# Optimization experiments

Hardware: AMD Instinct MI355X
Metric: run time of the kernel (lower is better)

## Reference

```python
import jax, jax.numpy as jnp
import numpy as np


def setup_inputs() -> dict:
    key = jax.random.key(0)
    feats = jax.random.normal(key, (16, 64, 128, 128), dtype=jnp.float32)
    return {"feats": feats, "stride": 2}


def reference(feats, stride):
    # Zero-insertion upsampling: equivalent to conv_transpose2d with an
    # s x s kernel whose only nonzero is at [0,0], stride=s, groups=C.
    # out[b,c,i*s,j*s] = feats[b,c,i,j]; all other entries are zero.
    B, C, H, W = feats.shape
    out = jnp.zeros((B, C, H * stride, W * stride), dtype=feats.dtype)
    out = out.at[:, :, ::stride, ::stride].set(feats)
    return out
```

## Files before the change

kernel.cpp:

```cpp
#include <hip/hip_runtime.h>


#define IN_H 128
#define IN_W 128
#define OUT_H 256
#define OUT_W 256

__global__ __launch_bounds__(256) void pad_within_kernel(
    const float* __restrict__ in, float* __restrict__ out) {
    unsigned v = blockIdx.x * blockDim.x + threadIdx.x;

    unsigned col4 = v & 63u;
    unsigned row  = v >> 6;
    unsigned oh   = row & 255u;
    unsigned bc   = row >> 8;

    float4 val;
    if (oh & 1u) {
        val = make_float4(0.f, 0.f, 0.f, 0.f);
    } else {
        const float2* irow =
            (const float2*)(in + ((size_t)bc * IN_H + (oh >> 1)) * IN_W);
        float2 x = irow[col4];
        val = make_float4(x.x, 0.f, x.y, 0.f);
    }
    ((float4*)out)[v] = val;
}

extern "C" void kernel_launch(void* const* d_in, const int* in_sizes, int n_in,
                              void* d_out, int out_size, void* d_ws, size_t ws_size,
                              hipStream_t stream) {
    const float* feats = (const float*)d_in[0];
    float* out = (float*)d_out;
    unsigned n_vec4 = (unsigned)(out_size / 4);
    dim3 block(256);
    dim3 grid(n_vec4 / 256);
    pad_within_kernel<<<grid, block, 0, stream>>>(feats, out);
}
```

Measured before the change: 299.8 us.

## Use grid-stride wave loop over row pairs with nontemporal loads and stores

Switches from one thread per output float4 to a persistent grid of 2048 blocks in which each wavefront handles one input row and writes both the data row and the zero row that follows it. Loads and stores use nontemporal builtins so the streamed output is meant to bypass cache retention. The intent is to drop per-thread index math and the odd/even branch, and to cut the launch to a fixed grid. The cost is a smaller grid that relies on the unrolled loop to keep enough memory requests in flight.

```diff
diff --git a/kernel.cpp b/kernel.cpp
--- a/kernel.cpp
+++ b/kernel.cpp
@@ -1,30 +1,31 @@
 #include <hip/hip_runtime.h>
 
 
-#define IN_H 128
-#define IN_W 128
-#define OUT_H 256
-#define OUT_W 256
+#define IN_W   128
+#define PAIRS  (16 * 64 * 128)
+
+typedef float f2 __attribute__((ext_vector_type(2)));
+typedef float f4 __attribute__((ext_vector_type(4)));
 
 __global__ __launch_bounds__(256) void pad_within_kernel(
     const float* __restrict__ in, float* __restrict__ out) {
-    unsigned v = blockIdx.x * blockDim.x + threadIdx.x;
+    const unsigned lane = threadIdx.x & 63u;
+    const unsigned wid  = (blockIdx.x * blockDim.x + threadIdx.x) >> 6;
+    const unsigned nw   = (gridDim.x * blockDim.x) >> 6;
 
-    unsigned col4 = v & 63u;
-    unsigned row  = v >> 6;
-    unsigned oh   = row & 255u;
-    unsigned bc   = row >> 8;
+    const f4 zero = {0.f, 0.f, 0.f, 0.f};
 
-    float4 val;
-    if (oh & 1u) {
-        val = make_float4(0.f, 0.f, 0.f, 0.f);
-    } else {
-        const float2* irow =
-            (const float2*)(in + ((size_t)bc * IN_H + (oh >> 1)) * IN_W);
-        float2 x = irow[col4];
-        val = make_float4(x.x, 0.f, x.y, 0.f);
+    #pragma unroll 4
+    for (unsigned p = wid; p < PAIRS; p += nw) {
+        const f2* irow = (const f2*)(in + (size_t)p * IN_W);
+        f2 x = __builtin_nontemporal_load(&irow[lane]);
+
+        f4 val = {x.x, 0.f, x.y, 0.f};
+
+        f4* opair = (f4*)(out + (size_t)p * 512);
+        __builtin_nontemporal_store(val,  &opair[lane]);
+        __builtin_nontemporal_store(zero, &opair[64u + lane]);
     }
-    ((float4*)out)[v] = val;
 }
 
 extern "C" void kernel_launch(void* const* d_in, const int* in_sizes, int n_in,
@@ -32,8 +33,7 @@
                               hipStream_t stream) {
     const float* feats = (const float*)d_in[0];
     float* out = (float*)d_out;
-    unsigned n_vec4 = (unsigned)(out_size / 4);
     dim3 block(256);
-    dim3 grid(n_vec4 / 256);
+    dim3 grid(2048);
     pad_within_kernel<<<grid, block, 0, stream>>>(feats, out);
 }
```

Result: slower. 309.5 us (+3.2%).
